# Optimization experiments

Measured on AMD Instinct MI355X. Metric: run time of the kernel, lower is better.

The kernel has to match this reference:

```python
import jax, jax.numpy as jnp
import numpy as np

B = 65536

def setup_inputs() -> dict:
    key = jax.random.key(0)
    ks = jax.random.split(key, 6)
    x = jax.random.normal(ks[0], (B, 784), dtype=jnp.float32)
    w_conv = jnp.ones((3, 3), dtype=jnp.float32)  # Parameter(ones((3,3)))
    w1 = jax.random.normal(ks[1], (676, 256), dtype=jnp.float32) * 0.04
    b1 = jax.random.normal(ks[2], (256,), dtype=jnp.float32) * 0.01
    w2 = jax.random.normal(ks[3], (256, 10), dtype=jnp.float32) * 0.06
    b2 = jax.random.normal(ks[4], (10,), dtype=jnp.float32) * 0.01
    return {"x": x, "w_conv": w_conv, "w1": w1, "b1": b1, "w2": w2, "b2": b2}

def reference(x, w_conv, w1, b1, w2, b2):
    b = x.shape[0]
    img = x.reshape(b, 1, 28, 28)
    # Convolve() is cross-correlation (no kernel flip), 'VALID': 28->26
    kern = w_conv.reshape(1, 1, 3, 3)
    conv = jax.lax.conv_general_dilated(
        img, kern, window_strides=(1, 1), padding='VALID',
        dimension_numbers=('NCHW', 'OIHW', 'NCHW'))  # (B,1,26,26)
    feat = conv.reshape(b, 676)
    h = jax.nn.relu(feat @ w1 + b1)  # (B,256)
    return h @ w2 + b2               # (B,10)
```

## Files before the change

### kernel.cpp

```cpp
#include <hip/hip_runtime.h>
#include <hip/hip_bf16.h>
#include <stdint.h>

typedef __bf16 bf16;
typedef __attribute__((ext_vector_type(8))) __bf16 bf16x8;
typedef __attribute__((ext_vector_type(4))) float f32x4;

#define KREAL 784
#define NTILES 25
#define TROW   32
#define TILE_ELEMS (256 * TROW)

__global__ __launch_bounds__(256) void prep_w1tt(const float* __restrict__ w_conv,
                                                 const float* __restrict__ w1,
                                                 bf16* __restrict__ W) {
    const int tile = blockIdx.x >> 5;
    const int kk   = blockIdx.x & 31;
    const int n    = threadIdx.x;
    const int k    = tile * 32 + kk;
    float s = 0.0f;
    if (k < KREAL) {
        const int r = k / 28, c = k % 28;
        #pragma unroll
        for (int di = 0; di < 3; ++di) {
            const int i = r - di;
            if (i < 0 || i >= 26) continue;
            #pragma unroll
            for (int dj = 0; dj < 3; ++dj) {
                const int j = c - dj;
                if (j < 0 || j >= 26) continue;
                s += w_conv[di * 3 + dj] * w1[(i * 26 + j) * 256 + n];
            }
        }
    }
    W[(size_t)tile * TILE_ELEMS + n * TROW + kk] = (bf16)s;
}

__global__ __launch_bounds__(256, 2) void fused_mlp(
    const float* __restrict__ x,
    const bf16*  __restrict__ W,
    const float* __restrict__ b1,
    const float* __restrict__ w2,
    const float* __restrict__ b2,
    float* __restrict__ out)
{
    __shared__ float w2s[256][10];
    __shared__ float b1s[256];
    __shared__ float b2s[10];

    const int t    = threadIdx.x;
    const int wave = t >> 6;
    const int lane = t & 63;
    const int c    = lane & 15;
    const int q    = lane >> 4;

    const int row0 = blockIdx.x * 128;

    for (int i = t; i < 2560; i += 256) ((float*)w2s)[i] = w2[i];
    b1s[t] = b1[t];
    if (t < 10) b2s[t] = b2[t];

    const float* arow0 = x + (size_t)(row0 + wave * 32 + c) * KREAL + q * 8;
    const float* arow1 = arow0 + (size_t)16 * KREAL;
    const bf16* wl = W + c * TROW + q * 8;

    f32x4 acc[2][16];
    #pragma unroll
    for (int mt = 0; mt < 2; ++mt)
        #pragma unroll
        for (int nt = 0; nt < 16; ++nt)
            acc[mt][nt] = (f32x4){0.f, 0.f, 0.f, 0.f};

    float4 f0a = *(const float4*)arow0, f0b = *(const float4*)(arow0 + 4);
    float4 f1a = *(const float4*)arow1, f1b = *(const float4*)(arow1 + 4);
    bf16x8 a0, a1;
    a0[0] = (bf16)f0a.x; a0[1] = (bf16)f0a.y; a0[2] = (bf16)f0a.z; a0[3] = (bf16)f0a.w;
    a0[4] = (bf16)f0b.x; a0[5] = (bf16)f0b.y; a0[6] = (bf16)f0b.z; a0[7] = (bf16)f0b.w;
    a1[0] = (bf16)f1a.x; a1[1] = (bf16)f1a.y; a1[2] = (bf16)f1a.z; a1[3] = (bf16)f1a.w;
    a1[4] = (bf16)f1b.x; a1[5] = (bf16)f1b.y; a1[6] = (bf16)f1b.z; a1[7] = (bf16)f1b.w;

    #pragma unroll 1
    for (int it = 0; it < NTILES; ++it) {
        const bool more = (it + 1) < NTILES;

        if (more) {
            const int kn = (it + 1) * 32;
            if (kn + q * 8 < KREAL) {
                const float* p0 = arow0 + kn;
                const float* p1 = arow1 + kn;
                f0a = *(const float4*)p0; f0b = *(const float4*)(p0 + 4);
                f1a = *(const float4*)p1; f1b = *(const float4*)(p1 + 4);
            } else {
                f0a = f0b = f1a = f1b = (float4){0.f, 0.f, 0.f, 0.f};
            }
        }

        const bf16* wt = wl + (size_t)it * TILE_ELEMS;
        #pragma unroll
        for (int nt = 0; nt < 16; ++nt) {
            bf16x8 b = *(const bf16x8*)(wt + nt * 16 * TROW);
            acc[0][nt] = __builtin_amdgcn_mfma_f32_16x16x32_bf16(a0, b, acc[0][nt], 0, 0, 0);
            acc[1][nt] = __builtin_amdgcn_mfma_f32_16x16x32_bf16(a1, b, acc[1][nt], 0, 0, 0);
        }

        if (more) {
            a0[0] = (bf16)f0a.x; a0[1] = (bf16)f0a.y; a0[2] = (bf16)f0a.z; a0[3] = (bf16)f0a.w;
            a0[4] = (bf16)f0b.x; a0[5] = (bf16)f0b.y; a0[6] = (bf16)f0b.z; a0[7] = (bf16)f0b.w;
            a1[0] = (bf16)f1a.x; a1[1] = (bf16)f1a.y; a1[2] = (bf16)f1a.z; a1[3] = (bf16)f1a.w;
            a1[4] = (bf16)f1b.x; a1[5] = (bf16)f1b.y; a1[6] = (bf16)f1b.z; a1[7] = (bf16)f1b.w;
        }
    }

    __syncthreads();

    float bl[16];
    #pragma unroll
    for (int nt = 0; nt < 16; ++nt) bl[nt] = b1s[nt * 16 + c];

    #pragma unroll
    for (int mt = 0; mt < 2; ++mt)
        #pragma unroll
        for (int nt = 0; nt < 16; ++nt)
            #pragma unroll
            for (int r = 0; r < 4; ++r) {
                float v = acc[mt][nt][r] + bl[nt];
                acc[mt][nt][r] = v > 0.f ? v : 0.f;
            }

    #pragma unroll 1
    for (int j = 0; j < 10; ++j) {
        float wj[16];
        #pragma unroll
        for (int nt = 0; nt < 16; ++nt) wj[nt] = w2s[nt * 16 + c][j];
        const float b2j = b2s[j];
        #pragma unroll
        for (int mt = 0; mt < 2; ++mt)
            #pragma unroll
            for (int r = 0; r < 4; ++r) {
                float s = 0.f;
                #pragma unroll
                for (int nt = 0; nt < 16; ++nt) s += acc[mt][nt][r] * wj[nt];
                s += __shfl_xor(s, 1, 64);
                s += __shfl_xor(s, 2, 64);
                s += __shfl_xor(s, 4, 64);
                s += __shfl_xor(s, 8, 64);
                if (c == j) {
                    const int row = row0 + wave * 32 + mt * 16 + q * 4 + r;
                    out[(size_t)row * 10 + j] = s + b2j;
                }
            }
    }
}

extern "C" void kernel_launch(void* const* d_in, const int* in_sizes, int n_in,
                              void* d_out, int out_size, void* d_ws, size_t ws_size,
                              hipStream_t stream) {
    const float* x  = (const float*)d_in[0];
    const float* wc = (const float*)d_in[1];
    const float* w1 = (const float*)d_in[2];
    const float* b1 = (const float*)d_in[3];
    const float* w2 = (const float*)d_in[4];
    const float* b2 = (const float*)d_in[5];
    float* out = (float*)d_out;
    bf16* W = (bf16*)d_ws;

    prep_w1tt<<<dim3(NTILES * 32), dim3(256), 0, stream>>>(wc, w1, W);
    fused_mlp<<<dim3(65536 / 128), dim3(256), 0, stream>>>(x, W, b1, w2, b2, out);
}
```

Before: 386.3 us.

## Split hidden dim across waves with 64-row blocks and register-prefetched B tiles

Changes the work split so each block handles 64 rows and each wave owns a 64-column slice of the hidden layer, with every wave using all 4 row tiles. The W tile for the next k-step is double-buffered in registers and the loop is unrolled by two. The second-layer partial sums are reduced with DPP adds instead of shuffles and combined across waves through shared memory. This is meant to cut the number of W loads per MFMA and raise the block count for occupancy. The cost is that each wave now loads every x row, so x traffic per block goes up fourfold, and a cross-wave shared-memory reduction is added.

```diff
diff --git a/kernel.cpp b/kernel.cpp
--- a/kernel.cpp
+++ b/kernel.cpp
@@ -36,6 +36,21 @@
     W[(size_t)tile * TILE_ELEMS + n * TROW + kk] = (bf16)s;
 }
 
+template <int CTRL>
+__device__ __forceinline__ float dpp_add(float s) {
+    int v = __builtin_amdgcn_update_dpp(0, __float_as_int(s), CTRL, 0xf, 0xf, false);
+    return s + __int_as_float(v);
+}
+
+__device__ __forceinline__ bf16x8 cvt8(float4 lo, float4 hi, float m) {
+    bf16x8 r;
+    r[0] = (bf16)(lo.x * m); r[1] = (bf16)(lo.y * m);
+    r[2] = (bf16)(lo.z * m); r[3] = (bf16)(lo.w * m);
+    r[4] = (bf16)(hi.x * m); r[5] = (bf16)(hi.y * m);
+    r[6] = (bf16)(hi.z * m); r[7] = (bf16)(hi.w * m);
+    return r;
+}
+
 __global__ __launch_bounds__(256, 2) void fused_mlp(
     const float* __restrict__ x,
     const bf16*  __restrict__ W,
@@ -44,9 +59,7 @@
     const float* __restrict__ b2,
     float* __restrict__ out)
 {
-    __shared__ float w2s[256][10];
-    __shared__ float b1s[256];
-    __shared__ float b2s[10];
+    __shared__ float part[4096];
 
     const int t    = threadIdx.x;
     const int wave = t >> 6;
@@ -54,101 +67,128 @@
     const int c    = lane & 15;
     const int q    = lane >> 4;
 
-    const int row0 = blockIdx.x * 128;
-
-    for (int i = t; i < 2560; i += 256) ((float*)w2s)[i] = w2[i];
-    b1s[t] = b1[t];
-    if (t < 10) b2s[t] = b2[t];
-
-    const float* arow0 = x + (size_t)(row0 + wave * 32 + c) * KREAL + q * 8;
-    const float* arow1 = arow0 + (size_t)16 * KREAL;
-    const bf16* wl = W + c * TROW + q * 8;
-
-    f32x4 acc[2][16];
-    #pragma unroll
-    for (int mt = 0; mt < 2; ++mt)
-        #pragma unroll
-        for (int nt = 0; nt < 16; ++nt)
+    const int row0 = blockIdx.x * 64;
+
+    const float* ar = x + (size_t)(row0 + c) * KREAL + q * 8;
+    const bf16* bp = W + (wave * 64 + c) * TROW + q * 8;
+
+    f32x4 acc[4][4];
+    #pragma unroll
+    for (int mt = 0; mt < 4; ++mt)
+        #pragma unroll
+        for (int nt = 0; nt < 4; ++nt)
             acc[mt][nt] = (f32x4){0.f, 0.f, 0.f, 0.f};
 
-    float4 f0a = *(const float4*)arow0, f0b = *(const float4*)(arow0 + 4);
-    float4 f1a = *(const float4*)arow1, f1b = *(const float4*)(arow1 + 4);
-    bf16x8 a0, a1;
-    a0[0] = (bf16)f0a.x; a0[1] = (bf16)f0a.y; a0[2] = (bf16)f0a.z; a0[3] = (bf16)f0a.w;
-    a0[4] = (bf16)f0b.x; a0[5] = (bf16)f0b.y; a0[6] = (bf16)f0b.z; a0[7] = (bf16)f0b.w;
-    a1[0] = (bf16)f1a.x; a1[1] = (bf16)f1a.y; a1[2] = (bf16)f1a.z; a1[3] = (bf16)f1a.w;
-    a1[4] = (bf16)f1b.x; a1[5] = (bf16)f1b.y; a1[6] = (bf16)f1b.z; a1[7] = (bf16)f1b.w;
+    float4 fa[4], fb[4];
+    bf16x8 a[4], BX[4], BY[4];
+
+    #pragma unroll
+    for (int mt = 0; mt < 4; ++mt) {
+        const float* p = ar + (size_t)(mt * 16) * KREAL;
+        fa[mt] = *(const float4*)p;
+        fb[mt] = *(const float4*)(p + 4);
+    }
+    #pragma unroll
+    for (int nt = 0; nt < 4; ++nt)
+        BX[nt] = *(const bf16x8*)(bp + nt * 512);
+    #pragma unroll
+    for (int mt = 0; mt < 4; ++mt) a[mt] = cvt8(fa[mt], fb[mt], 1.f);
+
+#define KSTEP(IT, BC, BN)                                                      \
+    do {                                                                       \
+        const bool more_ = (IT) + 1 < NTILES;                                  \
+        float okm_ = 1.f;                                                      \
+        if (more_) {                                                           \
+            const int kn_   = ((IT) + 1) * 32;                                 \
+            const bool ok_  = (kn_ + q * 8) < KREAL;   \
+            okm_ = ok_ ? 1.f : 0.f;                                            \
+            const int koff_ = ok_ ? kn_ : 0;                                   \
+            _Pragma("unroll")                                                  \
+            for (int mt = 0; mt < 4; ++mt) {             \
+                const float* p_ = ar + (size_t)(mt * 16) * KREAL + koff_;      \
+                fa[mt] = *(const float4*)p_;                                   \
+                fb[mt] = *(const float4*)(p_ + 4);                             \
+            }                                                                  \
+            const bf16* bt_ = bp + (size_t)((IT) + 1) * TILE_ELEMS;            \
+            _Pragma("unroll")                                                  \
+            for (int nt = 0; nt < 4; ++nt)              \
+                BN[nt] = *(const bf16x8*)(bt_ + nt * 512);                     \
+        }                                                                      \
+        _Pragma("unroll")                                                      \
+        for (int nt = 0; nt < 4; ++nt)                     \
+            _Pragma("unroll")                                                  \
+            for (int mt = 0; mt < 4; ++mt)                                     \
+                acc[mt][nt] = __builtin_amdgcn_mfma_f32_16x16x32_bf16(         \
+                    a[mt], BC[nt], acc[mt][nt], 0, 0, 0);                      \
+        if (more_) {                                          \
+            _Pragma("unroll")                                                  \
+            for (int mt = 0; mt < 4; ++mt) a[mt] = cvt8(fa[mt], fb[mt], okm_); \
+        }                                                                      \
+    } while (0)
 
     #pragma unroll 1
-    for (int it = 0; it < NTILES; ++it) {
-        const bool more = (it + 1) < NTILES;
-
-        if (more) {
-            const int kn = (it + 1) * 32;
-            if (kn + q * 8 < KREAL) {
-                const float* p0 = arow0 + kn;
-                const float* p1 = arow1 + kn;
-                f0a = *(const float4*)p0; f0b = *(const float4*)(p0 + 4);
-                f1a = *(const float4*)p1; f1b = *(const float4*)(p1 + 4);
-            } else {
-                f0a = f0b = f1a = f1b = (float4){0.f, 0.f, 0.f, 0.f};
-            }
-        }
-
-        const bf16* wt = wl + (size_t)it * TILE_ELEMS;
-        #pragma unroll
-        for (int nt = 0; nt < 16; ++nt) {
-            bf16x8 b = *(const bf16x8*)(wt + nt * 16 * TROW);
-            acc[0][nt] = __builtin_amdgcn_mfma_f32_16x16x32_bf16(a0, b, acc[0][nt], 0, 0, 0);
-            acc[1][nt] = __builtin_amdgcn_mfma_f32_16x16x32_bf16(a1, b, acc[1][nt], 0, 0, 0);
-        }
-
-        if (more) {
-            a0[0] = (bf16)f0a.x; a0[1] = (bf16)f0a.y; a0[2] = (bf16)f0a.z; a0[3] = (bf16)f0a.w;
-            a0[4] = (bf16)f0b.x; a0[5] = (bf16)f0b.y; a0[6] = (bf16)f0b.z; a0[7] = (bf16)f0b.w;
-            a1[0] = (bf16)f1a.x; a1[1] = (bf16)f1a.y; a1[2] = (bf16)f1a.z; a1[3] = (bf16)f1a.w;
-            a1[4] = (bf16)f1b.x; a1[5] = (bf16)f1b.y; a1[6] = (bf16)f1b.z; a1[7] = (bf16)f1b.w;
-        }
-    }
-
-    __syncthreads();
-
-    float bl[16];
-    #pragma unroll
-    for (int nt = 0; nt < 16; ++nt) bl[nt] = b1s[nt * 16 + c];
-
-    #pragma unroll
-    for (int mt = 0; mt < 2; ++mt)
-        #pragma unroll
-        for (int nt = 0; nt < 16; ++nt)
+    for (int base = 0; base < NTILES - 1; base += 2) {
+        KSTEP(base,     BX, BY);
+        KSTEP(base + 1, BY, BX);
+    }
+    KSTEP(NTILES - 1, BX, BY);
+#undef KSTEP
+
+    float bl[4];
+    #pragma unroll
+    for (int nt = 0; nt < 4; ++nt) bl[nt] = b1[wave * 64 + nt * 16 + c];
+
+    #pragma unroll
+    for (int mt = 0; mt < 4; ++mt)
+        #pragma unroll
+        for (int nt = 0; nt < 4; ++nt)
             #pragma unroll
             for (int r = 0; r < 4; ++r) {
                 float v = acc[mt][nt][r] + bl[nt];
                 acc[mt][nt][r] = v > 0.f ? v : 0.f;
             }
 
+    float keep[4][4];
+    #pragma unroll
+    for (int mt = 0; mt < 4; ++mt)
+        #pragma unroll
+        for (int r = 0; r < 4; ++r) keep[mt][r] = 0.f;
+
     #pragma unroll 1
     for (int j = 0; j < 10; ++j) {
-        float wj[16];
-        #pragma unroll
-        for (int nt = 0; nt < 16; ++nt) wj[nt] = w2s[nt * 16 + c][j];
-        const float b2j = b2s[j];
-        #pragma unroll
-        for (int mt = 0; mt < 2; ++mt)
+        float wj[4];
+        #pragma unroll
+        for (int nt = 0; nt < 4; ++nt) wj[nt] = w2[(wave * 64 + nt * 16 + c) * 10 + j];
+        #pragma unroll
+        for (int mt = 0; mt < 4; ++mt)
             #pragma unroll
             for (int r = 0; r < 4; ++r) {
                 float s = 0.f;
                 #pragma unroll
-                for (int nt = 0; nt < 16; ++nt) s += acc[mt][nt][r] * wj[nt];
-                s += __shfl_xor(s, 1, 64);
-                s += __shfl_xor(s, 2, 64);
-                s += __shfl_xor(s, 4, 64);
-                s += __shfl_xor(s, 8, 64);
-                if (c == j) {
-                    const int row = row0 + wave * 32 + mt * 16 + q * 4 + r;
-                    out[(size_t)row * 10 + j] = s + b2j;
-                }
+                for (int nt = 0; nt < 4; ++nt) s += acc[mt][nt][r] * wj[nt];
+                s = dpp_add<0xB1>(s);
+                s = dpp_add<0x4E>(s);
+                s = dpp_add<0x124>(s);
+                s = dpp_add<0x128>(s);
+                if (c == j) keep[mt][r] = s;
             }
+    }
+
+    #pragma unroll
+    for (int mt = 0; mt < 4; ++mt)
+        #pragma unroll
+        for (int r = 0; r < 4; ++r)
+            if (c < 10)
+                part[((((wave * 4 + mt) * 4 + r) * 4 + q) << 4) + c] = keep[mt][r];
+    __syncthreads();
+    for (int idx = t; idx < 640; idx += 256) {
+        const int row = idx / 10, cc = idx - row * 10;
+        const int mt = row >> 4, qq = (row >> 2) & 3, rr = row & 3;
+        float s = b2[cc];
+        #pragma unroll
+        for (int nh = 0; nh < 4; ++nh)
+            s += part[((((nh * 4 + mt) * 4 + rr) * 4 + qq) << 4) + cc];
+        out[(size_t)(row0 + row) * 10 + cc] = s;
     }
 }
 
@@ -165,5 +205,5 @@
     bf16* W = (bf16*)d_ws;
 
     prep_w1tt<<<dim3(NTILES * 32), dim3(256), 0, stream>>>(wc, w1, W);
-    fused_mlp<<<dim3(65536 / 128), dim3(256), 0, stream>>>(x, W, b1, w2, b2, out);
-}
+    fused_mlp<<<dim3(65536 / 64), dim3(256), 0, stream>>>(x, W, b1, w2, b2, out);
+}
```

Result: faster. 371.4 us (-3.9%).
